# Kernel tuning notes

Hardware: AMD Instinct MI355X
Metric: run time of the kernel (lower is better)

Reference implementation:

```python
import jax, jax.numpy as jnp
import numpy as np

B, Q, T, H, M, K, V = 4, 1024, 1024, 16, 1024, 64, 64


def _masked_softmax(logits, active, axis):
    # jnp softmax(..., where=active, initial=0.0): max taken over active entries
    # with initial value 0.0; inactive positions get probability 0.
    neg = jnp.where(active, logits, -jnp.inf)
    m = jnp.maximum(jnp.max(neg, axis=axis, keepdims=True), 0.0)
    e = jnp.where(active, jnp.exp(neg - m), 0.0)
    return e / jnp.sum(e, axis=axis, keepdims=True)


def _entropy_bits(p, where, axis):
    # entropy in bits over `axis`, counting only `where` entries; 0*log0 -> 0
    mask = (where > 0) & (p > 0)
    pl = jnp.where(mask, p * jnp.log2(jnp.where(mask, p, 1.0)), 0.0)
    return -jnp.sum(pl, axis=axis)


def setup_inputs() -> dict:
    key = jax.random.key(0)
    k1, k2, k3, k4, k5, k6 = jax.random.split(key, 6)
    mscale = 1.0 / np.sqrt(M)
    vscale = 1.0 / np.sqrt(V)
    qinput = jax.random.normal(k1, (B, Q, M), jnp.float32)
    kvinput = jax.random.normal(k2, (B, T, M), jnp.float32)
    qmask = jnp.zeros((B, Q), jnp.float32)
    tmask = jnp.zeros((B, T), jnp.float32)
    # causal combined mask: 1 = ignore future target positions
    qtmask = jnp.broadcast_to(jnp.triu(jnp.ones((Q, T), jnp.float32), k=1), (B, Q, T))
    wq = jax.random.normal(k3, (H, M, K), jnp.float32) * mscale
    wk = jax.random.normal(k4, (H, M, K), jnp.float32) * mscale
    wv = jax.random.normal(k5, (H, M, V), jnp.float32) * mscale
    wo = jax.random.normal(k6, (H, V, M), jnp.float32) * vscale
    return {"qinput": qinput, "kvinput": kvinput, "qmask": qmask, "tmask": tmask,
            "qtmask": qtmask, "wq": wq, "wk": wk, "wv": wv, "wo": wo}


def reference(qinput, kvinput, qmask, tmask, qtmask, wq, wk, wv, wo):
    kscale = 1.0 / np.sqrt(K)
    qm = qmask[:, :, None]                      # bq1
    tm = tmask[:, None, :]                      # b1t
    logits_mask = jnp.maximum(tm, qtmask)       # bqt, 1 = ignore

    query = jnp.einsum('hmd,bqm->bhqd', wq, qinput)
    key_ = jnp.einsum('hmd,btm->bhtd', wk, kvinput)
    val = jnp.einsum('hmd,btm->bhtd', wv, kvinput)

    alogit = jnp.einsum('bhqd,bhtd->bhqt', query, key_)
    active = (1.0 - logits_mask)[:, None, :, :] > 0          # bhqt (broadcast)
    att = _masked_softmax(alogit * kscale, active, axis=3)   # bhqt

    # attention entropy statistics
    occu = 1.0 - logits_mask                                  # bqt
    row_occu = jnp.sum(occu, axis=2, keepdims=True)[:, None, :, :]  # b1q1
    active_cols = jnp.max(occu, axis=1)                       # bt
    target_marg = jnp.sum(att * row_occu, axis=(1, 2))        # bt
    target_sum = jnp.sum(target_marg, axis=1, keepdims=True)
    target_norm = target_marg / target_sum
    target_entr = _entropy_bits(target_norm, active_cols, axis=1)  # b
    c = jnp.sum(active_cols, axis=1)
    scaled_entr = target_entr / jnp.log2(c)

    pre = jnp.einsum('bhqt,bhtd->bhqd', att, val)
    out = jnp.einsum('hdm,bhqd->bqm', wo, pre)
    out = out * (1.0 - qm)
    return (out, scaled_entr)
```

## Files before the change

kernel.cpp:

```cpp
#include <hip/hip_runtime.h>
#include <hip/hip_bf16.h>

typedef unsigned short u16;
typedef __attribute__((ext_vector_type(8))) short bf16x8;
typedef __attribute__((ext_vector_type(4))) float f32x4;

#define MFMA(a, b, c) __builtin_amdgcn_mfma_f32_16x16x32_bf16(a, b, c, 0, 0, 0)

__device__ inline u16 f2bf(float f) {
    union { __hip_bfloat16 b; u16 u; } cv;
    cv.b = __float2bfloat16(f);
    return cv.u;
}

__device__ inline f32x4 zero4() {
    f32x4 v; v[0] = 0.f; v[1] = 0.f; v[2] = 0.f; v[3] = 0.f; return v;
}

__device__ inline void gl_lds16(const u16* g, u16* l) {
    __builtin_amdgcn_global_load_lds(
        (const __attribute__((address_space(1))) u16*)(g),
        (__attribute__((address_space(3))) u16*)(l), 16, 0, 0);
}

__device__ inline void barrier_nodrain() {
    asm volatile("s_waitcnt lgkmcnt(0)\ns_barrier" ::: "memory");
}

__global__ __launch_bounds__(256) void prep_kernel(const float* __restrict__ qa, const float* __restrict__ kva,
                                                   u16* __restrict__ oq, u16* __restrict__ okv,
                                                   const float* __restrict__ wq, const float* __restrict__ wk,
                                                   const float* __restrict__ wv, const float* __restrict__ wo,
                                                   u16* __restrict__ W3, u16* __restrict__ Wot,
                                                   float* __restrict__ marg) {
    __shared__ float tile[64][65];
    int bid = blockIdx.x, tid = threadIdx.x;
    if (bid >= 9216) {
        for (int i = tid; i < 4096; i += 256) marg[i] = 0.f;
        return;
    }
    if (bid < 8192) {
        const float* in = (bid < 4096) ? qa : kva;
        u16* out = (bid < 4096) ? oq : okv;
        int i = (((bid & 4095) * 256) + tid) * 4;
        float4 v = *(const float4*)(in + i);
        u16 o[4] = { f2bf(v.x), f2bf(v.y), f2bf(v.z), f2bf(v.w) };
        *(uint2*)(out + i) = *(const uint2*)o;
        return;
    }
    int v_ = bid - 8192;
    int bx = v_ & 15, by = (v_ >> 4) & 3, h = v_ >> 6;
    const float* src; u16* dst; int R, C, ho, r0, c0;
    if (by == 3) { src = wo; dst = Wot; R = 64; C = 1024; ho = 64; r0 = 0; c0 = bx * 64; }
    else {
        src = (by == 0) ? wq : (by == 1) ? wk : wv;
        dst = W3 + (size_t)by * 1024 * 1024;
        R = 1024; C = 64; ho = 64 * 1024; r0 = bx * 64; c0 = 0;
    }
    const float* s = src + (size_t)h * R * C;
#pragma unroll
    for (int k = 0; k < 16; k++) {
        int idx = tid + k * 256;
        int i = idx >> 6, j = idx & 63;
        tile[i][j] = s[(size_t)(r0 + i) * C + (c0 + j)];
    }
    __syncthreads();
    u16* d = dst + (size_t)h * ho;
#pragma unroll
    for (int k = 0; k < 16; k++) {
        int idx = tid + k * 256;
        int j = idx >> 6, i = idx & 63;
        d[(size_t)(c0 + j) * 1024 + (r0 + i)] = f2bf(tile[i][j]);
    }
}

#define QSC 0.18033688011112042f

__global__ __launch_bounds__(256) void proj_kernel(const u16* __restrict__ Xq, const u16* __restrict__ Xkv,
                                                   const u16* __restrict__ W3,
                                                   u16* __restrict__ Qp, u16* __restrict__ Kp,
                                                   u16* __restrict__ Vt) {
    __shared__ __align__(16) u16 As[128 * 32];
    __shared__ __align__(16) u16 Bs[128 * 32];
    __shared__ __align__(16) u16 Ts[128 * 136];
    int tid = threadIdx.x;
    int ny = blockIdx.y;
    int sel = ny >> 3;
    const u16* A  = (sel == 0) ? Xq : Xkv;
    const u16* Bt = W3 + (size_t)sel * 1024 * 1024;
    int m0 = blockIdx.x * 128, n0 = (ny & 7) * 128;
    int w = tid >> 6, lane = tid & 63, quad = lane >> 4, c = lane & 15;
    int mw = (w & 1) * 64, nw = (w >> 1) * 64;
    f32x4 acc[4][4];
#pragma unroll
    for (int i = 0; i < 4; i++)
#pragma unroll
        for (int j = 0; j < 4; j++) acc[i][j] = zero4();

    for (int k0 = 0; k0 < 1024; k0 += 32) {
        __syncthreads();
#pragma unroll
        for (int s = 0; s < 2; s++) {
            int ch = s * 256 + w * 64 + lane;
            int r = ch >> 2, cc = (ch & 3) * 8;
            gl_lds16(&A[(size_t)(m0 + r) * 1024 + k0 + cc],  &As[(s * 256 + w * 64) * 8]);
            gl_lds16(&Bt[(size_t)(n0 + r) * 1024 + k0 + cc], &Bs[(s * 256 + w * 64) * 8]);
        }
        asm volatile("s_waitcnt vmcnt(0)" ::: "memory");
        __syncthreads();
        bf16x8 af[4], bfr[4];
#pragma unroll
        for (int i = 0; i < 4; i++) af[i] = *(const bf16x8*)&As[(mw + i * 16 + c) * 32 + quad * 8];
#pragma unroll
        for (int j = 0; j < 4; j++) bfr[j] = *(const bf16x8*)&Bs[(nw + j * 16 + c) * 32 + quad * 8];
#pragma unroll
        for (int i = 0; i < 4; i++)
#pragma unroll
            for (int j = 0; j < 4; j++) acc[i][j] = MFMA(af[i], bfr[j], acc[i][j]);
    }
    if (sel < 2) {
        u16* C_ = (sel == 0) ? Qp : Kp;
        float scl = (sel == 0) ? QSC : 1.0f;
#pragma unroll
        for (int i = 0; i < 4; i++)
#pragma unroll
            for (int r = 0; r < 4; r++) {
                int row = m0 + mw + i * 16 + quad * 4 + r;
#pragma unroll
                for (int j = 0; j < 4; j++)
                    C_[(size_t)row * 1024 + n0 + nw + j * 16 + c] = f2bf(acc[i][j][r] * scl);
            }
    } else {
#pragma unroll
        for (int i = 0; i < 4; i++)
#pragma unroll
            for (int r = 0; r < 4; r++) {
                int rowL = mw + i * 16 + quad * 4 + r;
#pragma unroll
                for (int j = 0; j < 4; j++)
                    Ts[(nw + j * 16 + c) * 136 + rowL] = f2bf(acc[i][j][r]);
            }
        __syncthreads();
        int bb = m0 >> 10, tbase = m0 & 1023;
#pragma unroll
        for (int it = 0; it < 8; it++) {
            int linear = tid + it * 256;
            int colL = linear >> 4, r0 = (linear & 15) * 8;
            int colG = n0 + colL;
            bf16x8 v = *(const bf16x8*)&Ts[colL * 136 + r0];
            *(bf16x8*)&Vt[(((size_t)(bb * 16 + (colG >> 6)) * 64) + (colG & 63)) * 1024 + tbase + r0] = v;
        }
    }
}

__global__ __launch_bounds__(256) void gemmo_kernel(const u16* __restrict__ A, const u16* __restrict__ Bt,
                                                    float* __restrict__ Cf, const float* __restrict__ qmask) {
    __shared__ __align__(16) u16 As[128 * 32];
    __shared__ __align__(16) u16 Bs[128 * 32];
    int tid = threadIdx.x;
    int m0 = blockIdx.x * 128, n0 = blockIdx.y * 128;
    int w = tid >> 6, lane = tid & 63, quad = lane >> 4, c = lane & 15;
    int mw = (w & 1) * 64, nw = (w >> 1) * 64;
    f32x4 acc[4][4];
#pragma unroll
    for (int i = 0; i < 4; i++)
#pragma unroll
        for (int j = 0; j < 4; j++) acc[i][j] = zero4();

    for (int k0 = 0; k0 < 1024; k0 += 32) {
        __syncthreads();
#pragma unroll
        for (int s = 0; s < 2; s++) {
            int ch = s * 256 + w * 64 + lane;
            int r = ch >> 2, cc = (ch & 3) * 8;
            gl_lds16(&A[(size_t)(m0 + r) * 1024 + k0 + cc],  &As[(s * 256 + w * 64) * 8]);
            gl_lds16(&Bt[(size_t)(n0 + r) * 1024 + k0 + cc], &Bs[(s * 256 + w * 64) * 8]);
        }
        asm volatile("s_waitcnt vmcnt(0)" ::: "memory");
        __syncthreads();
        bf16x8 af[4], bfr[4];
#pragma unroll
        for (int i = 0; i < 4; i++) af[i] = *(const bf16x8*)&As[(mw + i * 16 + c) * 32 + quad * 8];
#pragma unroll
        for (int j = 0; j < 4; j++) bfr[j] = *(const bf16x8*)&Bs[(nw + j * 16 + c) * 32 + quad * 8];
#pragma unroll
        for (int i = 0; i < 4; i++)
#pragma unroll
            for (int j = 0; j < 4; j++) acc[i][j] = MFMA(af[i], bfr[j], acc[i][j]);
    }
#pragma unroll
    for (int i = 0; i < 4; i++) {
#pragma unroll
        for (int r = 0; r < 4; r++) {
            int row = m0 + mw + i * 16 + quad * 4 + r;
            float scale = 1.0f - qmask[row];
#pragma unroll
            for (int j = 0; j < 4; j++) {
                int col = n0 + nw + j * 16 + c;
                Cf[(size_t)row * 1024 + col] = acc[i][j][r] * scale;
            }
        }
    }
}

__global__ __launch_bounds__(512) void attn_kernel(const u16* __restrict__ Qp, const u16* __restrict__ Kp,
                                                   const u16* __restrict__ Vt, u16* __restrict__ Pre,
                                                   float* __restrict__ marg) {
    __shared__ __align__(16) u16 Ks[2][64 * 64];
    __shared__ __align__(16) u16 Vs[2][64 * 64];
    __shared__ __align__(16) u16 plds[8][16 * 72];
    float* colbuf = (float*)&Vs[0][0];
    float* wrbuf  = (float*)&plds[0][0];
    int tid = threadIdx.x;
    int bid = blockIdx.x;
    int k2 = bid >> 6;
    int m = (k2 & 1) ? (7 - (k2 >> 1)) : (k2 >> 1);
    int g = bid & 63;
    int h = g & 15, b = g >> 4;
    int bx = m;
    int nA = 16 - bx, nB = bx + 1;
    int w = tid >> 6, lane = tid & 63, quad = lane >> 4, c = lane & 15;

    int nq = (w < 4) ? nA : nB;
    int q0 = (w < 4) ? ((15 - bx) * 64 + w * 16) : (bx * 64 + (w - 4) * 16);

    const u16* qrow = Qp + (size_t)(b * 1024 + q0 + c) * 1024 + h * 64;
    bf16x8 aq0 = *(const bf16x8*)(qrow + quad * 8);
    bf16x8 aq1 = *(const bf16x8*)(qrow + 32 + quad * 8);

    const u16* kb = Kp + (size_t)b * 1024 * 1024 + h * 64;
    const u16* vb = Vt + (size_t)(b * 16 + h) * 64 * 1024;
    u16* pl = plds[w];

    int rowS = tid >> 3;
    int lu = (tid & 7) ^ (rowS & 7);
    int sw = c & 7;
    int su0 = (quad ^ sw) * 8;
    int su1 = ((quad ^ 4) ^ sw) * 8;
    u16* ldsK = &Ks[0][0] + w * 512;
    u16* ldsV = &Vs[0][0] + w * 512;

    f32x4 o[4];
#pragma unroll
    for (int i = 0; i < 4; i++) o[i] = zero4();
    float lsum = 0.f;
    int qg[4];
#pragma unroll
    for (int r = 0; r < 4; r++) qg[r] = q0 + quad * 4 + r;

    gl_lds16(kb + (size_t)rowS * 1024 + lu * 8, ldsK);
    gl_lds16(vb + (size_t)rowS * 1024 + lu * 8, ldsV);
    for (int ci = 0; ci < nA; ci++) {
        int bf = ci & 1;
        barrier_nodrain();
        if (ci + 1 < nA) {
            gl_lds16(kb + (size_t)((ci + 1) * 64 + rowS) * 1024 + lu * 8, ldsK + (bf ^ 1) * 4096);
            gl_lds16(vb + (size_t)rowS * 1024 + (ci + 1) * 64 + lu * 8,  ldsV + (bf ^ 1) * 4096);
            asm volatile("s_waitcnt vmcnt(2)" ::: "memory");
        } else {
            asm volatile("s_waitcnt vmcnt(0)" ::: "memory");
        }
        asm volatile("s_barrier" ::: "memory");
        if (ci < nq) {
            const u16* Kb = &Ks[bf][0];
            const u16* Vb = &Vs[bf][0];
            f32x4 sT[4];
#pragma unroll
            for (int j = 0; j < 4; j++) {
                const u16* kr = Kb + (j * 16 + c) * 64;
                sT[j] = MFMA(*(const bf16x8*)(kr + su0), aq0, zero4());
                sT[j] = MFMA(*(const bf16x8*)(kr + su1), aq1, sT[j]);
            }
            if (ci < nq - 1) {
#pragma unroll
                for (int j = 0; j < 4; j++) {
                    u16 tmp[4];
#pragma unroll
                    for (int r = 0; r < 4; r++) {
                        float e = exp2f(sT[j][r]);
                        lsum += e;
                        tmp[r] = f2bf(e);
                    }
                    *(uint2*)&pl[c * 72 + j * 16 + quad * 4] = *(const uint2*)tmp;
                }
            } else {
                int qq = q0 + c;
#pragma unroll
                for (int j = 0; j < 4; j++) {
                    int tl = ci * 64 + j * 16 + quad * 4;
                    u16 tmp[4];
#pragma unroll
                    for (int r = 0; r < 4; r++) {
                        float e = (tl + r <= qq) ? exp2f(sT[j][r]) : 0.f;
                        lsum += e;
                        tmp[r] = f2bf(e);
                    }
                    *(uint2*)&pl[c * 72 + j * 16 + quad * 4] = *(const uint2*)tmp;
                }
            }
            asm volatile("s_waitcnt lgkmcnt(0)" ::: "memory");
            bf16x8 ap0 = *(const bf16x8*)&pl[c * 72 + quad * 8];
            bf16x8 ap1 = *(const bf16x8*)&pl[c * 72 + 32 + quad * 8];
#pragma unroll
            for (int vt = 0; vt < 4; vt++) {
                const u16* vr = Vb + (vt * 16 + c) * 64;
                o[vt] = MFMA(ap0, *(const bf16x8*)(vr + su0), o[vt]);
                o[vt] = MFMA(ap1, *(const bf16x8*)(vr + su1), o[vt]);
            }
        }
    }

    lsum += __shfl_xor(lsum, 16);
    lsum += __shfl_xor(lsum, 32);
    float invc = 1.0f / lsum;
    float invl[4];
#pragma unroll
    for (int r = 0; r < 4; r++) invl[r] = __shfl(invc, quad * 4 + r);
#pragma unroll
    for (int vt = 0; vt < 4; vt++)
#pragma unroll
        for (int r = 0; r < 4; r++) {
            size_t row = (size_t)(b * 1024 + q0 + quad * 4 + r);
            Pre[row * 1024 + h * 64 + vt * 16 + c] = f2bf(o[vt][r] * invl[r]);
        }

    float wr[4];
#pragma unroll
    for (int r = 0; r < 4; r++) wr[r] = (float)(qg[r] + 1) * invl[r];

    bf16x8 aqH0 = aq0, aqH1 = aq1;
    int q0H = q0;
    if (w >= 4) {
        q0H = (15 - bx) * 64 + (w - 4) * 16;
        const u16* qrowH = Qp + (size_t)(b * 1024 + q0H + c) * 1024 + h * 64;
        aqH0 = *(const bf16x8*)(qrowH + quad * 8);
        aqH1 = *(const bf16x8*)(qrowH + 32 + quad * 8);
    }
    asm volatile("s_waitcnt vmcnt(0)" ::: "memory");
    __syncthreads();
    if (c == 0) {
#pragma unroll
        for (int r = 0; r < 4; r++) wrbuf[w * 16 + quad * 4 + r] = wr[r];
    }
    gl_lds16(kb + (size_t)rowS * 1024 + lu * 8, ldsK);
    for (int i = tid; i < nA * 64; i += 512) colbuf[i] = 0.f;
    __syncthreads();
    float wrH[4];
    int qgH[4];
#pragma unroll
    for (int r = 0; r < 4; r++) {
        qgH[r] = q0H + quad * 4 + r;
        wrH[r] = (w < 4) ? wr[r] : wrbuf[(w - 4) * 16 + quad * 4 + r];
    }

    for (int ci = 0; ci < nA; ci++) {
        int bf = ci & 1;
        barrier_nodrain();
        if (ci + 1 < nA) {
            gl_lds16(kb + (size_t)((ci + 1) * 64 + rowS) * 1024 + lu * 8, ldsK + (bf ^ 1) * 4096);
            asm volatile("s_waitcnt vmcnt(1)" ::: "memory");
        } else {
            asm volatile("s_waitcnt vmcnt(0)" ::: "memory");
        }
        asm volatile("s_barrier" ::: "memory");
        const u16* Kb = &Ks[bf][0];
        if (ci < nB) {
            f32x4 s[4];
#pragma unroll
            for (int j = 0; j < 4; j++) {
                const u16* kr = Kb + (j * 16 + c) * 64;
                s[j] = MFMA(aq0, *(const bf16x8*)(kr + su0), zero4());
                s[j] = MFMA(aq1, *(const bf16x8*)(kr + su1), s[j]);
            }
            bool diag = (w >= 4) && (ci == nB - 1);
            float a[4];
#pragma unroll
            for (int j = 0; j < 4; j++) {
                int t = ci * 64 + j * 16 + c;
                float aj = 0.f;
#pragma unroll
                for (int r = 0; r < 4; r++) {
                    float term = exp2f(s[j][r]) * wr[r];
                    aj += (!diag || t <= qg[r]) ? term : 0.f;
                }
                aj += __shfl_xor(aj, 16);
                aj += __shfl_xor(aj, 32);
                a[j] = aj;
            }
            float v = (quad == 0) ? a[0] : (quad == 1) ? a[1] : (quad == 2) ? a[2] : a[3];
            atomicAdd(&colbuf[ci * 64 + lane], v);
        } else {
            int jb = (w >= 4) ? 2 : 0;
            f32x4 s2[2];
#pragma unroll
            for (int jj = 0; jj < 2; jj++) {
                const u16* kr = Kb + ((jb + jj) * 16 + c) * 64;
                s2[jj] = MFMA(aqH0, *(const bf16x8*)(kr + su0), zero4());
                s2[jj] = MFMA(aqH1, *(const bf16x8*)(kr + su1), s2[jj]);
            }
            bool diag = (ci == nA - 1);
            float a2[2];
#pragma unroll
            for (int jj = 0; jj < 2; jj++) {
                int t = ci * 64 + (jb + jj) * 16 + c;
                float aj = 0.f;
#pragma unroll
                for (int r = 0; r < 4; r++) {
                    float term = exp2f(s2[jj][r]) * wrH[r];
                    aj += (!diag || t <= qgH[r]) ? term : 0.f;
                }
                aj += __shfl_xor(aj, 16);
                aj += __shfl_xor(aj, 32);
                a2[jj] = aj;
            }
            float v = (quad == 0) ? a2[0] : a2[1];
            if (quad < 2) atomicAdd(&colbuf[ci * 64 + (jb + quad) * 16 + c], v);
        }
    }
    __syncthreads();
    for (int t = tid; t < nA * 64; t += 512) atomicAdd(&marg[b * 1024 + t], colbuf[t]);
}

__global__ __launch_bounds__(256) void entropy_kernel(const float* __restrict__ marg, float* __restrict__ out) {
    int b = blockIdx.x, tid = threadIdx.x;
    __shared__ float red[256];
    float s = 0.f;
    for (int t = tid; t < 1024; t += 256) s += marg[b * 1024 + t];
    red[tid] = s; __syncthreads();
    for (int k = 128; k > 0; k >>= 1) { if (tid < k) red[tid] += red[tid + k]; __syncthreads(); }
    float tot = red[0];
    __syncthreads();
    float e = 0.f;
    for (int t = tid; t < 1024; t += 256) {
        float p = marg[b * 1024 + t] / tot;
        if (p > 0.f) e -= p * log2f(p);
    }
    red[tid] = e; __syncthreads();
    for (int k = 128; k > 0; k >>= 1) { if (tid < k) red[tid] += red[tid + k]; __syncthreads(); }
    if (tid == 0) out[b] = red[0] * 0.1f;
}

extern "C" void kernel_launch(void* const* d_in, const int* in_sizes, int n_in,
                              void* d_out, int out_size, void* d_ws, size_t ws_size,
                              hipStream_t stream) {
    const float* qinput  = (const float*)d_in[0];
    const float* kvinput = (const float*)d_in[1];
    const float* qmask   = (const float*)d_in[2];
    const float* wq = (const float*)d_in[5];
    const float* wk = (const float*)d_in[6];
    const float* wv = (const float*)d_in[7];
    const float* wo = (const float*)d_in[8];

    char* ws = (char*)d_ws;
    const size_t MB = 1024 * 1024;
    u16* Xq   = (u16*)(ws + 0);
    u16* Xkv  = (u16*)(ws + 8 * MB);
    u16* W3   = (u16*)(ws + 16 * MB);
    u16* Wot  = (u16*)(ws + 22 * MB);
    u16* Qp   = (u16*)(ws + 24 * MB);
    u16* Kp   = (u16*)(ws + 32 * MB);
    u16* Vt   = (u16*)(ws + 40 * MB);
    float* marg = (float*)(ws + 48 * MB);
    u16* Pre = Xq;
    float* out = (float*)d_out;

    prep_kernel<<<9217, 256, 0, stream>>>(qinput, kvinput, Xq, Xkv, wq, wk, wv, wo, W3, Wot, marg);
    proj_kernel<<<dim3(32, 24), 256, 0, stream>>>(Xq, Xkv, W3, Qp, Kp, Vt);

    attn_kernel<<<512, 512, 0, stream>>>(Qp, Kp, Vt, Pre, marg);
    gemmo_kernel<<<dim3(32, 8), 256, 0, stream>>>(Pre, Wot, out, qmask);
    entropy_kernel<<<4, 256, 0, stream>>>(marg, out + (size_t)4 * 1024 * 1024);
}
```

Measured before the change: 216.5 us.

## Fuse K and V projections per block and fold entropy into output GEMM

```diff
diff --git a/kernel.cpp b/kernel.cpp
--- a/kernel.cpp
+++ b/kernel.cpp
@@ -76,26 +76,29 @@
 
 #define QSC 0.18033688011112042f
 
-__global__ __launch_bounds__(256) void proj_kernel(const u16* __restrict__ Xq, const u16* __restrict__ Xkv,
-                                                   const u16* __restrict__ W3,
-                                                   u16* __restrict__ Qp, u16* __restrict__ Kp,
-                                                   u16* __restrict__ Vt) {
-    __shared__ __align__(16) u16 As[128 * 32];
-    __shared__ __align__(16) u16 Bs[128 * 32];
-    __shared__ __align__(16) u16 Ts[128 * 136];
+__global__ __launch_bounds__(256, 2) void proj_kernel(const u16* __restrict__ Xq, const u16* __restrict__ Xkv,
+                                                      const u16* __restrict__ W3,
+                                                      u16* __restrict__ Qp, u16* __restrict__ Kp,
+                                                      u16* __restrict__ Vt) {
+    __shared__ __align__(16) union ShM {
+        struct { u16 As[128 * 32]; u16 B0[128 * 32]; u16 B1[128 * 32]; } d;
+        u16 Ts[128 * 136];
+    } sh;
     int tid = threadIdx.x;
-    int ny = blockIdx.y;
-    int sel = ny >> 3;
-    const u16* A  = (sel == 0) ? Xq : Xkv;
-    const u16* Bt = W3 + (size_t)sel * 1024 * 1024;
-    int m0 = blockIdx.x * 128, n0 = (ny & 7) * 128;
+    int bid = blockIdx.x;
+    int ny = bid & 15, mblk = bid >> 4;
+    int m0 = mblk * 128, n0 = (ny & 7) * 128;
+    bool isQ = (ny < 8);
+    const u16* Ap  = isQ ? Xq : Xkv;
+    const u16* BtK = W3 + (size_t)(isQ ? 0 : 1) * 1024 * 1024 + (size_t)n0 * 1024;
+    const u16* BtV = W3 + (size_t)2 * 1024 * 1024 + (size_t)n0 * 1024;
     int w = tid >> 6, lane = tid & 63, quad = lane >> 4, c = lane & 15;
     int mw = (w & 1) * 64, nw = (w >> 1) * 64;
-    f32x4 acc[4][4];
+    f32x4 acc0[4][4], acc1[4][4];
 #pragma unroll
     for (int i = 0; i < 4; i++)
 #pragma unroll
-        for (int j = 0; j < 4; j++) acc[i][j] = zero4();
+        for (int j = 0; j < 4; j++) { acc0[i][j] = zero4(); acc1[i][j] = zero4(); }
 
     for (int k0 = 0; k0 < 1024; k0 += 32) {
         __syncthreads();
@@ -103,24 +106,32 @@
         for (int s = 0; s < 2; s++) {
             int ch = s * 256 + w * 64 + lane;
             int r = ch >> 2, cc = (ch & 3) * 8;
-            gl_lds16(&A[(size_t)(m0 + r) * 1024 + k0 + cc],  &As[(s * 256 + w * 64) * 8]);
-            gl_lds16(&Bt[(size_t)(n0 + r) * 1024 + k0 + cc], &Bs[(s * 256 + w * 64) * 8]);
+            gl_lds16(&Ap[(size_t)(m0 + r) * 1024 + k0 + cc],  &sh.d.As[(s * 256 + w * 64) * 8]);
+            gl_lds16(&BtK[(size_t)r * 1024 + k0 + cc],        &sh.d.B0[(s * 256 + w * 64) * 8]);
+            if (!isQ) gl_lds16(&BtV[(size_t)r * 1024 + k0 + cc], &sh.d.B1[(s * 256 + w * 64) * 8]);
         }
         asm volatile("s_waitcnt vmcnt(0)" ::: "memory");
         __syncthreads();
-        bf16x8 af[4], bfr[4];
-#pragma unroll
-        for (int i = 0; i < 4; i++) af[i] = *(const bf16x8*)&As[(mw + i * 16 + c) * 32 + quad * 8];
-#pragma unroll
-        for (int j = 0; j < 4; j++) bfr[j] = *(const bf16x8*)&Bs[(nw + j * 16 + c) * 32 + quad * 8];
+        bf16x8 af[4], bf0[4];
+#pragma unroll
+        for (int i = 0; i < 4; i++) af[i] = *(const bf16x8*)&sh.d.As[(mw + i * 16 + c) * 32 + quad * 8];
+#pragma unroll
+        for (int j = 0; j < 4; j++) bf0[j] = *(const bf16x8*)&sh.d.B0[(nw + j * 16 + c) * 32 + quad * 8];
 #pragma unroll
         for (int i = 0; i < 4; i++)
 #pragma unroll
-            for (int j = 0; j < 4; j++) acc[i][j] = MFMA(af[i], bfr[j], acc[i][j]);
-    }
-    if (sel < 2) {
-        u16* C_ = (sel == 0) ? Qp : Kp;
-        float scl = (sel == 0) ? QSC : 1.0f;
+            for (int j = 0; j < 4; j++) acc0[i][j] = MFMA(af[i], bf0[j], acc0[i][j]);
+        if (!isQ) {
+            bf16x8 bf1[4];
+#pragma unroll
+            for (int j = 0; j < 4; j++) bf1[j] = *(const bf16x8*)&sh.d.B1[(nw + j * 16 + c) * 32 + quad * 8];
+#pragma unroll
+            for (int i = 0; i < 4; i++)
+#pragma unroll
+                for (int j = 0; j < 4; j++) acc1[i][j] = MFMA(af[i], bf1[j], acc1[i][j]);
+        }
+    }
+    if (isQ) {
 #pragma unroll
         for (int i = 0; i < 4; i++)
 #pragma unroll
@@ -128,9 +139,19 @@
                 int row = m0 + mw + i * 16 + quad * 4 + r;
 #pragma unroll
                 for (int j = 0; j < 4; j++)
-                    C_[(size_t)row * 1024 + n0 + nw + j * 16 + c] = f2bf(acc[i][j][r] * scl);
+                    Qp[(size_t)row * 1024 + n0 + nw + j * 16 + c] = f2bf(acc0[i][j][r] * QSC);
             }
     } else {
+#pragma unroll
+        for (int i = 0; i < 4; i++)
+#pragma unroll
+            for (int r = 0; r < 4; r++) {
+                int row = m0 + mw + i * 16 + quad * 4 + r;
+#pragma unroll
+                for (int j = 0; j < 4; j++)
+                    Kp[(size_t)row * 1024 + n0 + nw + j * 16 + c] = f2bf(acc0[i][j][r]);
+            }
+        __syncthreads();
 #pragma unroll
         for (int i = 0; i < 4; i++)
 #pragma unroll
@@ -138,7 +159,7 @@
                 int rowL = mw + i * 16 + quad * 4 + r;
 #pragma unroll
                 for (int j = 0; j < 4; j++)
-                    Ts[(nw + j * 16 + c) * 136 + rowL] = f2bf(acc[i][j][r]);
+                    sh.Ts[(nw + j * 16 + c) * 136 + rowL] = f2bf(acc1[i][j][r]);
             }
         __syncthreads();
         int bb = m0 >> 10, tbase = m0 & 1023;
@@ -147,18 +168,39 @@
             int linear = tid + it * 256;
             int colL = linear >> 4, r0 = (linear & 15) * 8;
             int colG = n0 + colL;
-            bf16x8 v = *(const bf16x8*)&Ts[colL * 136 + r0];
+            bf16x8 v = *(const bf16x8*)&sh.Ts[colL * 136 + r0];
             *(bf16x8*)&Vt[(((size_t)(bb * 16 + (colG >> 6)) * 64) + (colG & 63)) * 1024 + tbase + r0] = v;
         }
     }
 }
 
 __global__ __launch_bounds__(256) void gemmo_kernel(const u16* __restrict__ A, const u16* __restrict__ Bt,
-                                                    float* __restrict__ Cf, const float* __restrict__ qmask) {
+                                                    float* __restrict__ Cf, const float* __restrict__ qmask,
+                                                    const float* __restrict__ marg, float* __restrict__ entr) {
     __shared__ __align__(16) u16 As[128 * 32];
     __shared__ __align__(16) u16 Bs[128 * 32];
+    __shared__ float red[256];
     int tid = threadIdx.x;
-    int m0 = blockIdx.x * 128, n0 = blockIdx.y * 128;
+    int bid = blockIdx.x;
+    if (bid >= 256) {
+        int b = bid - 256;
+        float s = 0.f;
+        for (int t = tid; t < 1024; t += 256) s += marg[b * 1024 + t];
+        red[tid] = s; __syncthreads();
+        for (int k = 128; k > 0; k >>= 1) { if (tid < k) red[tid] += red[tid + k]; __syncthreads(); }
+        float tot = red[0];
+        __syncthreads();
+        float e = 0.f;
+        for (int t = tid; t < 1024; t += 256) {
+            float p = marg[b * 1024 + t] / tot;
+            if (p > 0.f) e -= p * log2f(p);
+        }
+        red[tid] = e; __syncthreads();
+        for (int k = 128; k > 0; k >>= 1) { if (tid < k) red[tid] += red[tid + k]; __syncthreads(); }
+        if (tid == 0) entr[b] = red[0] * 0.1f;
+        return;
+    }
+    int m0 = (bid >> 3) * 128, n0 = (bid & 7) * 128;
     int w = tid >> 6, lane = tid & 63, quad = lane >> 4, c = lane & 15;
     int mw = (w & 1) * 64, nw = (w >> 1) * 64;
     f32x4 acc[4][4];
@@ -421,25 +463,6 @@
     for (int t = tid; t < nA * 64; t += 512) atomicAdd(&marg[b * 1024 + t], colbuf[t]);
 }
 
-__global__ __launch_bounds__(256) void entropy_kernel(const float* __restrict__ marg, float* __restrict__ out) {
-    int b = blockIdx.x, tid = threadIdx.x;
-    __shared__ float red[256];
-    float s = 0.f;
-    for (int t = tid; t < 1024; t += 256) s += marg[b * 1024 + t];
-    red[tid] = s; __syncthreads();
-    for (int k = 128; k > 0; k >>= 1) { if (tid < k) red[tid] += red[tid + k]; __syncthreads(); }
-    float tot = red[0];
-    __syncthreads();
-    float e = 0.f;
-    for (int t = tid; t < 1024; t += 256) {
-        float p = marg[b * 1024 + t] / tot;
-        if (p > 0.f) e -= p * log2f(p);
-    }
-    red[tid] = e; __syncthreads();
-    for (int k = 128; k > 0; k >>= 1) { if (tid < k) red[tid] += red[tid + k]; __syncthreads(); }
-    if (tid == 0) out[b] = red[0] * 0.1f;
-}
-
 extern "C" void kernel_launch(void* const* d_in, const int* in_sizes, int n_in,
                               void* d_out, int out_size, void* d_ws, size_t ws_size,
                               hipStream_t stream) {
@@ -465,9 +488,8 @@
     float* out = (float*)d_out;
 
     prep_kernel<<<9217, 256, 0, stream>>>(qinput, kvinput, Xq, Xkv, wq, wk, wv, wo, W3, Wot, marg);
-    proj_kernel<<<dim3(32, 24), 256, 0, stream>>>(Xq, Xkv, W3, Qp, Kp, Vt);
+    proj_kernel<<<512, 256, 0, stream>>>(Xq, Xkv, W3, Qp, Kp, Vt);
 
     attn_kernel<<<512, 512, 0, stream>>>(Qp, Kp, Vt, Pre, marg);
-    gemmo_kernel<<<dim3(32, 8), 256, 0, stream>>>(Pre, Wot, out, qmask);
-    entropy_kernel<<<4, 256, 0, stream>>>(marg, out + (size_t)4 * 1024 * 1024);
-}
+    gemmo_kernel<<<260, 256, 0, stream>>>(Pre, Wot, out, qmask, marg, out + (size_t)4 * 1024 * 1024);
+}
```

New measurement: 214.5 us. No clear change (-0.9%).
